# Kernel optimization log

Measured on AMD Instinct MI355X. Metric: run time of the kernel, lower is better.

Reference implementation:

```python
import jax, jax.numpy as jnp
from jax import lax
import numpy as np

B = 256
# conv stack: (in_ch, out_ch, kernel)
_CONV_CFG = [(1, 3, 4), (3, 9, 4), (9, 12, 4), (12, 15, 4), (15, 15, 3)]
_FLAT = 15 * 4 ** 4  # 3840, matches nn.Linear(15*(18-14)**4, 100)


def _conv4d(x, w, b):
    """True 4D valid convolution. x: [B,C,d1,d2,d3,d4], w: [O,I,k,k,k,k]."""
    dn = lax.conv_dimension_numbers(x.shape, w.shape, ('NCDHWX', 'OIDHWX', 'NCDHWX'))
    y = lax.conv_general_dilated(x, w, window_strides=(1, 1, 1, 1),
                                 padding='VALID', dimension_numbers=dn)
    return y + b.reshape((1, -1) + (1,) * 4)


def setup_inputs() -> dict:
    key = jax.random.key(0)
    ks = jax.random.split(key, 16)
    inp = {'x': jax.random.normal(ks[0], (B, 1, 18, 18, 18, 18), dtype=jnp.float32)}
    for i, (ci, co, k) in enumerate(_CONV_CFG, start=1):
        fan_in = ci * k ** 4
        inp[f'w{i}'] = jax.random.normal(ks[2 * i - 1], (co, ci, k, k, k, k), dtype=jnp.float32) / np.sqrt(fan_in)
        inp[f'b{i}'] = jnp.zeros((co,), dtype=jnp.float32)
    inp['fc1_w'] = jax.random.normal(ks[11], (_FLAT, 100), dtype=jnp.float32) / np.sqrt(_FLAT)
    inp['fc1_b'] = jnp.zeros((100,), dtype=jnp.float32)
    inp['fc2_w'] = jax.random.normal(ks[12], (100, 1), dtype=jnp.float32) / np.sqrt(100.0)
    inp['fc2_b'] = jnp.zeros((1,), dtype=jnp.float32)
    return inp


def reference(x, w1, b1, w2, b2, w3, b3, w4, b4, w5, b5, fc1_w, fc1_b, fc2_w, fc2_b):
    h = jax.nn.relu(_conv4d(x, w1, b1))
    h = jax.nn.relu(_conv4d(h, w2, b2))
    h = jax.nn.relu(_conv4d(h, w3, b3))
    h = jax.nn.relu(_conv4d(h, w4, b4))
    h = jax.nn.relu(_conv4d(h, w5, b5))  # [B,15,4,4,4,4]
    h = h.reshape(h.shape[0], -1)        # [B,3840], torch Flatten order
    # Dropout(0.5) is identity at inference (eval mode)
    h = jax.nn.relu(h @ fc1_w + fc1_b)
    return jax.nn.sigmoid(h @ fc2_w + fc2_b)  # [B,1]
```

## Files before the change

kernel.cpp:

```cpp
#include <hip/hip_runtime.h>
#include <hip/hip_bf16.h>


#define BATCH 256
typedef unsigned int u32;
typedef float    f32x4  __attribute__((ext_vector_type(4)));
typedef float    f32x16 __attribute__((ext_vector_type(16)));
typedef _Float16 f16x8  __attribute__((ext_vector_type(8)));

struct __attribute__((packed, aligned(4))) f16x8w { f16x8 v; };

__global__ void cvt_f32_f16(const float* __restrict__ in, _Float16* __restrict__ o, int n8) {
    int i = blockIdx.x * blockDim.x + threadIdx.x;
    if (i >= n8) return;
    const f32x4* p = (const f32x4*)(in + (size_t)i * 8);
    f32x4 a = p[0], b = p[1];
    f16x8 v;
    #pragma unroll
    for (int j = 0; j < 4; ++j) { v[j] = (_Float16)a[j]; v[4 + j] = (_Float16)b[j]; }
    *(f16x8*)(o + (size_t)i * 8) = v;
}

template<int COUT, int CIN, int KS, int S>
__global__ void prepack_v5(const float* __restrict__ w, _Float16* __restrict__ wf) {
    constexpr int STEPS = CIN * KS * 2 * KS;
    constexpr int TOT = STEPS * 512;
    int idx = blockIdx.x * 256 + threadIdx.x;
    if (idx >= TOT) return;
    int j    = idx & 7;
    int lane = (idx >> 3) & 63;
    int st   = idx >> 9;
    int k1 = st % KS;
    int r1 = st / KS;
    int k3p = r1 & 1;
    int r2  = r1 >> 1;
    int k2 = r2 % KS;
    int ci = r2 / KS;
    int gg = lane >> 5, col = lane & 31;
    int oc = col / S, s = col % S;
    int k3 = k3p * 2 + gg;
    int k4 = j - s;
    float v = 0.0f;
    if (oc < COUT && k3 < KS && k4 >= 0 && k4 < KS)
        v = w[((((oc * CIN + ci) * KS + k1) * KS + k2) * KS + k3) * KS + k4];
    wf[idx] = (_Float16)v;
}

template<int BYTES>
__device__ __forceinline__ void stage_b(const _Float16* gsrc, char* ldst, int tid) {
    constexpr int N16 = BYTES / 16;
    const int wv = tid >> 6, ln = tid & 63;
    #pragma unroll
    for (int it = 0; it * 256 < N16; ++it) {
        int u16 = it * 256 + (wv << 6);
        if (u16 < N16) {
            const char* gp = (const char*)gsrc + (size_t)(u16 + ln) * 16;
            __builtin_amdgcn_global_load_lds(
                (const __attribute__((address_space(1))) unsigned int*)gp,
                (__attribute__((address_space(3))) unsigned int*)(ldst + u16 * 16),
                16, 0, 0);
        }
    }
}

template<int CIN, int COUT, int KS, int DIN, int DP, int S, int OP, int T, int CG>
__launch_bounds__(256, 4)
__global__ void conv4d_v5(const _Float16* __restrict__ x,
                          const _Float16* __restrict__ wf,
                          const float* __restrict__ bias,
                          _Float16* __restrict__ out) {
    constexpr int DOUT = DIN - KS + 1;
    constexpr int NB   = (DOUT + S - 1) / S;
    constexpr int PCOL = DOUT * DOUT * NB;
    constexpr int NTC  = (PCOL + 31) / 32;
    constexpr int NG   = DOUT / T;
    static_assert(DOUT % T == 0, "T must divide DOUT");
    constexpr int XD2 = DIN * DP;
    constexpr int XD1 = DIN * XD2;
    constexpr int XCI = DIN * XD1;
    constexpr int GROUPS = CIN * KS * 2;
    static_assert(GROUPS % CG == 0, "CG must divide GROUPS");
    constexpr int CSTEPS = CG * KS;
    constexpr int CBYTES = CSTEPS * 1024;
    constexpr int NCHUNK = GROUPS / CG;
    constexpr int AJ = T + KS - 1;
    constexpr u32 NW   = (u32)BATCH * NG * NTC;
    constexpr u32 POUT = (u32)DOUT * DOUT * DOUT * OP;

    __shared__ char bsm[2 * CBYTES];
    const int tid = threadIdx.x;
    u32 wid = blockIdx.x * 4u + (u32)(tid >> 6);
    if (wid >= NW) wid = NW - 1u;
    const int ln = tid & 63;
    const int g  = ln >> 5;
    const int r  = ln & 31;

    u32 tc = wid % (u32)NTC;  u32 q = wid / (u32)NTC;
    u32 d1g = q % (u32)NG;    u32 b = q / (u32)NG;
    u32 rr = tc * 32u + (u32)r;  if (rr >= (u32)PCOL) rr = (u32)PCOL - 1u;
    u32 u  = rr % (u32)NB;    u32 q2 = rr / (u32)NB;
    u32 d3 = q2 % (u32)DOUT;  u32 d2 = q2 / (u32)DOUT;

    const u32 lanebase2 = (b * (u32)(CIN * XCI) + d1g * (u32)(T * XD1)
                         + d2 * (u32)XD2 + d3 * (u32)DP + (u32)(g * DP)
                         + u * (u32)S) * 2u;
    const char* xc = (const char*)x;

    f32x16 acc[T];
    #pragma unroll
    for (int t = 0; t < T; ++t)
        #pragma unroll
        for (int i = 0; i < 16; ++i) acc[t][i] = 0.0f;

    stage_b<CBYTES>(wf, &bsm[0], tid);

    #pragma unroll 1
    for (int ch = 0; ch < NCHUNK; ++ch) {
        __syncthreads();
        if (ch + 1 < NCHUNK)
            stage_b<CBYTES>(wf + (size_t)(ch + 1) * CSTEPS * 512,
                            &bsm[((ch + 1) & 1) * CBYTES], tid);
        const char* bb = &bsm[(ch & 1) * CBYTES] + ln * 16;
        #pragma unroll
        for (int gi = 0; gi < CG; ++gi) {
            int grp = ch * CG + gi;
            int k3p = grp & 1;
            int k2  = (grp >> 1) % KS;
            int ci  = (grp >> 1) / KS;
            u32 goff = ((u32)ci * (u32)XCI + (u32)k2 * (u32)XD2
                      + (u32)(k3p * 2 * DP)) * 2u;
            const char* ap = xc + lanebase2 + goff;
            f16x8 ar[AJ];
            #pragma unroll
            for (int j = 0; j < AJ; ++j)
                ar[j] = ((const f16x8w*)(ap + j * (XD1 * 2)))->v;
            #pragma unroll
            for (int k1 = 0; k1 < KS; ++k1) {
                f16x8 bf = *(const f16x8*)(bb + (gi * KS + k1) * 1024);
                #pragma unroll
                for (int t = 0; t < T; ++t)
                    acc[t] = __builtin_amdgcn_mfma_f32_32x32x16_f16(ar[k1 + t], bf, acc[t], 0, 0, 0);
            }
        }
    }

    const int oc = r / S, s = r % S;
    if (oc >= COUT) return;
    float bv = bias[oc];
    #pragma unroll
    for (int t = 0; t < T; ++t) {
        u32 d1 = d1g * (u32)T + (u32)t;
        #pragma unroll
        for (int reg = 0; reg < 16; ++reg) {
            int rowoff = (reg & 3) + 8 * (reg >> 2) + 4 * g;
            u32 rr2 = tc * 32u + (u32)rowoff;
            if (rr2 >= (u32)PCOL) rr2 = (u32)PCOL - 1u;
            u32 uu = rr2 % (u32)NB;  u32 qq = rr2 / (u32)NB;
            u32 dd3 = qq % (u32)DOUT; u32 dd2 = qq / (u32)DOUT;
            u32 d4 = uu * (u32)S + (u32)s;
            if (d4 < (u32)DOUT) {
                u32 oidx = (b * (u32)COUT + (u32)oc) * POUT
                         + ((d1 * (u32)DOUT + dd2) * (u32)DOUT + dd3) * (u32)OP + d4;
                out[oidx] = (_Float16)fmaxf(acc[t][reg] + bv, 0.0f);
            }
        }
    }
}

__global__ void prepack_fc1(const float* __restrict__ w, _Float16* __restrict__ wf) {
    int idx = blockIdx.x * 256 + threadIdx.x;
    if (idx >= 430080) return;
    int j    = idx & 7;
    int lane = (idx >> 3) & 63;
    int t9   = idx >> 9;
    int st   = t9 % 120;
    int ni   = t9 / 120;
    int k    = st * 32 + (lane >> 4) * 8 + j;
    int col  = ni * 16 + (lane & 15);
    wf[idx] = (_Float16)((col < 100) ? w[k * 100 + col] : 0.0f);
}

__launch_bounds__(256)
__global__ void fc1_mfma(const _Float16* __restrict__ h,
                         const _Float16* __restrict__ wfc,
                         const float* __restrict__ bias,
                         float* __restrict__ o) {
    int wv   = blockIdx.x * 4 + (threadIdx.x >> 6);
    int lane = threadIdx.x & 63;
    int r = lane & 15, g = lane >> 4;
    int mi = wv / 7, ni = wv % 7;
    const f16x8* A  = (const f16x8*)(h + (size_t)(mi * 16 + r) * 3840);
    const f16x8* Bv = (const f16x8*)wfc;
    f32x4 acc = {0.f, 0.f, 0.f, 0.f};
    #pragma unroll 4
    for (int st = 0; st < 120; ++st) {
        f16x8 a = A[st * 4 + g];
        f16x8 b = Bv[(ni * 120 + st) * 64 + lane];
        acc = __builtin_amdgcn_mfma_f32_16x16x32_f16(a, b, acc, 0, 0, 0);
    }
    int col = ni * 16 + r;
    if (col < 100) {
        float bv = bias[col];
        #pragma unroll
        for (int i = 0; i < 4; ++i) {
            int row = mi * 16 + g * 4 + i;
            o[row * 100 + col] = fmaxf(acc[i] + bv, 0.0f);
        }
    }
}

__global__ void fc2_sigmoid(const float* __restrict__ h,
                            const float* __restrict__ w,
                            const float* __restrict__ bias,
                            float* __restrict__ out) {
    int b = blockIdx.x * blockDim.x + threadIdx.x;
    if (b >= BATCH) return;
    const float* hb = h + b * 100;
    float acc = bias[0];
    #pragma unroll
    for (int j = 0; j < 100; ++j)
        acc = fmaf(hb[j], w[j], acc);
    out[b] = 1.0f / (1.0f + expf(-acc));
}

extern "C" void kernel_launch(void* const* d_in, const int* in_sizes, int n_in,
                              void* d_out, int out_size, void* d_ws, size_t ws_size,
                              hipStream_t stream) {
    const float* x    = (const float*)d_in[0];
    const float* w1   = (const float*)d_in[1];
    const float* b1   = (const float*)d_in[2];
    const float* w2   = (const float*)d_in[3];
    const float* b2   = (const float*)d_in[4];
    const float* w3   = (const float*)d_in[5];
    const float* b3   = (const float*)d_in[6];
    const float* w4   = (const float*)d_in[7];
    const float* b4   = (const float*)d_in[8];
    const float* w5   = (const float*)d_in[9];
    const float* b5   = (const float*)d_in[10];
    const float* fc1w = (const float*)d_in[11];
    const float* fc1b = (const float*)d_in[12];
    const float* fc2w = (const float*)d_in[13];
    const float* fc2b = (const float*)d_in[14];
    float* out = (float*)d_out;

    _Float16* W = (_Float16*)d_ws;
    size_t cur = 0;
    auto alloc = [&](size_t n) { _Float16* p = W + cur; cur += (n + 255) & ~(size_t)255; return p; };
    _Float16* x16 = alloc(26873856);
    _Float16* h1  = alloc(41472000);
    _Float16* h2  = alloc(47775744);
    _Float16* h3  = alloc(22394880);
    _Float16* h4  = alloc(4976640);
    _Float16* h5  = alloc(983040);
    _Float16* wf1 = alloc(16384);
    _Float16* wf2 = alloc(49152);
    _Float16* wf3 = alloc(147456);
    _Float16* wf4 = alloc(196608);
    _Float16* wf5 = alloc(138240);
    _Float16* wfc = alloc(430080);
    float* fc1out = (float*)alloc(51200 + 256);

    cvt_f32_f16<<<13122, 256, 0, stream>>>(x, x16, 3359232);

    prepack_v5<3, 1, 4, 4><<<64,  256, 0, stream>>>(w1, wf1);
    prepack_v5<9, 3, 4, 2><<<192, 256, 0, stream>>>(w2, wf2);
    prepack_v5<12, 9, 4, 2><<<576, 256, 0, stream>>>(w3, wf3);
    prepack_v5<15, 12, 4, 2><<<768, 256, 0, stream>>>(w4, wf4);
    prepack_v5<15, 15, 3, 2><<<540, 256, 0, stream>>>(w5, wf5);
    prepack_fc1<<<1680, 256, 0, stream>>>(fc1w, wfc);

    conv4d_v5<1, 3, 4, 18, 18, 4, 16, 3, 4><<<9280, 256, 0, stream>>>(x16, wf1, b1, h1);
    conv4d_v5<3, 9, 4, 15, 16, 2, 12, 3, 4><<<6912, 256, 0, stream>>>(h1, wf2, b2, h2);
    conv4d_v5<9, 12, 4, 12, 12, 2, 10, 3, 4><<<2496, 256, 0, stream>>>(h2, wf3, b3, h3);
    conv4d_v5<12, 15, 4, 9, 10, 2, 6, 3, 4><<<512, 256, 0, stream>>>(h3, wf4, b4, h4);
    conv4d_v5<15, 15, 3, 6, 6, 2, 4, 4, 6><<<64, 256, 0, stream>>>(h4, wf5, b5, h5);

    fc1_mfma<<<28, 256, 0, stream>>>(h5, wfc, fc1b, fc1out);
    fc2_sigmoid<<<1, 256, 0, stream>>>(fc1out, fc2w, fc2b, out);
}
```

Before: 996.0 us.

## Add 2D output tiling conv kernel reusing A fragments across d1 and d2

Adds a new conv4d_v6 kernel that tiles the output over two spatial dims (T1×T2) so each warp's loaded A fragments are reused across both k1 and k2 shifts. It also reorders the weight prepacking so weight chunks are staged per (ci,k3 pair) group. The aim is fewer global activation loads per MFMA and fewer blocks. The first four conv layers switch to it with new tile sizes. The cost is more accumulator registers per warp and dropping the occupancy hint from launch bounds, which may lower occupancy or cause spills.

```diff
diff --git a/kernel.cpp b/kernel.cpp
--- a/kernel.cpp
+++ b/kernel.cpp
@@ -19,6 +19,30 @@
     #pragma unroll
     for (int j = 0; j < 4; ++j) { v[j] = (_Float16)a[j]; v[4 + j] = (_Float16)b[j]; }
     *(f16x8*)(o + (size_t)i * 8) = v;
+}
+
+template<int COUT, int CIN, int KS, int S>
+__global__ void prepack_v6(const float* __restrict__ w, _Float16* __restrict__ wf) {
+    constexpr int STEPS = CIN * 2 * KS * KS;
+    constexpr int TOT = STEPS * 512;
+    int idx = blockIdx.x * 256 + threadIdx.x;
+    if (idx >= TOT) return;
+    int j    = idx & 7;
+    int lane = (idx >> 3) & 63;
+    int st   = idx >> 9;
+    int k1  = st % KS;
+    int k2  = (st / KS) % KS;
+    int sgv = st / (KS * KS);
+    int k3p = sgv & 1;
+    int ci  = sgv >> 1;
+    int gg = lane >> 5, col = lane & 31;
+    int oc = col / S, s = col % S;
+    int k3 = k3p * 2 + gg;
+    int k4 = j - s;
+    float v = 0.0f;
+    if (oc < COUT && k3 < KS && k4 >= 0 && k4 < KS)
+        v = w[((((oc * CIN + ci) * KS + k1) * KS + k2) * KS + k3) * KS + k4];
+    wf[idx] = (_Float16)v;
 }
 
 template<int COUT, int CIN, int KS, int S>
@@ -63,6 +87,131 @@
     }
 }
 
+template<int CIN, int COUT, int KS, int DIN, int DP, int S, int OP,
+         int T1, int T2, int CG>
+__launch_bounds__(256)
+__global__ void conv4d_v6(const _Float16* __restrict__ x,
+                          const _Float16* __restrict__ wf,
+                          const float* __restrict__ bias,
+                          _Float16* __restrict__ out) {
+    constexpr int DOUT = DIN - KS + 1;
+    constexpr int NB   = (DOUT + S - 1) / S;
+    static_assert((BATCH * DOUT * NB) % 32 == 0, "M rows must tile by 32");
+    static_assert(DOUT % T1 == 0 && DOUT % T2 == 0, "T must divide DOUT");
+    constexpr int NTC = BATCH * DOUT * NB / 32;
+    constexpr int NG1 = DOUT / T1;
+    constexpr int NG2 = DOUT / T2;
+    constexpr int XD2 = DIN * DP;
+    constexpr int XD1 = DIN * XD2;
+    constexpr int XCI = DIN * XD1;
+    constexpr int SG  = CIN * 2;
+    static_assert(SG % CG == 0, "CG must divide SG");
+    constexpr int NCHUNK = SG / CG;
+    constexpr int CBYTES = CG * KS * KS * 1024;
+    constexpr int AJ1 = T1 + KS - 1;
+    constexpr int AJ2 = T2 + KS - 1;
+    constexpr u32 POUT = (u32)DOUT * DOUT * DOUT * OP;
+
+    __shared__ char bsm[2 * CBYTES];
+    const int tid = threadIdx.x;
+    const u32 wid = blockIdx.x * 4u + (u32)(tid >> 6);
+    const int ln = tid & 63;
+    const int g  = ln >> 5;
+    const int r  = ln & 31;
+
+    u32 tc = wid / (u32)(NG1 * NG2);
+    u32 rm = wid % (u32)(NG1 * NG2);
+    u32 g1 = rm / (u32)NG2;
+    u32 g2 = rm % (u32)NG2;
+
+    u32 rr = tc * 32u + (u32)r;
+    u32 u  = rr % (u32)NB;   u32 q = rr / (u32)NB;
+    u32 d3 = q % (u32)DOUT;  u32 bb = q / (u32)DOUT;
+
+    const u32 lanebase2 = (bb * (u32)(CIN * XCI) + g1 * (u32)(T1 * XD1)
+                         + g2 * (u32)(T2 * XD2) + d3 * (u32)DP + (u32)(g * DP)
+                         + u * (u32)S) * 2u;
+    const char* xc = (const char*)x;
+
+    f32x16 acc[T1][T2];
+    #pragma unroll
+    for (int t1 = 0; t1 < T1; ++t1)
+        #pragma unroll
+        for (int t2 = 0; t2 < T2; ++t2)
+            #pragma unroll
+            for (int i = 0; i < 16; ++i) acc[t1][t2][i] = 0.0f;
+
+    stage_b<CBYTES>(wf, &bsm[0], tid);
+
+    #pragma unroll 1
+    for (int ch = 0; ch < NCHUNK; ++ch) {
+        __syncthreads();
+        if (ch + 1 < NCHUNK)
+            stage_b<CBYTES>(wf + (size_t)(ch + 1) * (CBYTES / 2),
+                            &bsm[((ch + 1) & 1) * CBYTES], tid);
+        const char* bb_lds = &bsm[(ch & 1) * CBYTES] + ln * 16;
+        #pragma unroll
+        for (int cgi = 0; cgi < CG; ++cgi) {
+            int sg  = ch * CG + cgi;
+            int k3p = sg & 1;
+            int ci  = sg >> 1;
+            u32 sgoff = ((u32)ci * (u32)XCI + (u32)(k3p * 2) * (u32)DP) * 2u;
+            const char* ap = xc + lanebase2 + sgoff;
+
+            f16x8 fr[AJ1][AJ2];
+            #pragma unroll
+            for (int j2 = 0; j2 < T2 - 1; ++j2)
+                #pragma unroll
+                for (int j1 = 0; j1 < AJ1; ++j1)
+                    fr[j1][j2] = ((const f16x8w*)(ap + (j1 * XD1 + j2 * XD2) * 2))->v;
+
+            #pragma unroll
+            for (int k2 = 0; k2 < KS; ++k2) {
+                constexpr int dummy = 0; (void)dummy;
+                const int jc = k2 + T2 - 1;
+                #pragma unroll
+                for (int j1 = 0; j1 < AJ1; ++j1)
+                    fr[j1][jc] = ((const f16x8w*)(ap + (j1 * XD1 + jc * XD2) * 2))->v;
+                #pragma unroll
+                for (int k1 = 0; k1 < KS; ++k1) {
+                    f16x8 bf = *(const f16x8*)(bb_lds + ((cgi * KS + k2) * KS + k1) * 1024);
+                    #pragma unroll
+                    for (int t1 = 0; t1 < T1; ++t1)
+                        #pragma unroll
+                        for (int t2 = 0; t2 < T2; ++t2)
+                            acc[t1][t2] = __builtin_amdgcn_mfma_f32_32x32x16_f16(
+                                fr[k1 + t1][k2 + t2], bf, acc[t1][t2], 0, 0, 0);
+                }
+            }
+        }
+    }
+
+    const int oc = r / S, s = r % S;
+    if (oc >= COUT) return;
+    float bv = bias[oc];
+    #pragma unroll
+    for (int t1 = 0; t1 < T1; ++t1) {
+        u32 d1 = g1 * (u32)T1 + (u32)t1;
+        #pragma unroll
+        for (int t2 = 0; t2 < T2; ++t2) {
+            u32 d2 = g2 * (u32)T2 + (u32)t2;
+            #pragma unroll
+            for (int reg = 0; reg < 16; ++reg) {
+                int rowoff = (reg & 3) + 8 * (reg >> 2) + 4 * g;
+                u32 rr2 = tc * 32u + (u32)rowoff;
+                u32 uu = rr2 % (u32)NB;  u32 qq = rr2 / (u32)NB;
+                u32 dd3 = qq % (u32)DOUT; u32 bb2 = qq / (u32)DOUT;
+                u32 d4 = uu * (u32)S + (u32)s;
+                if (d4 < (u32)DOUT) {
+                    u32 oidx = (bb2 * (u32)COUT + (u32)oc) * POUT
+                             + ((d1 * (u32)DOUT + d2) * (u32)DOUT + dd3) * (u32)OP + d4;
+                    out[oidx] = (_Float16)fmaxf(acc[t1][t2][reg] + bv, 0.0f);
+                }
+            }
+        }
+    }
+}
+
 template<int CIN, int COUT, int KS, int DIN, int DP, int S, int OP, int T, int CG>
 __launch_bounds__(256, 4)
 __global__ void conv4d_v5(const _Float16* __restrict__ x,
@@ -262,17 +411,17 @@
 
     cvt_f32_f16<<<13122, 256, 0, stream>>>(x, x16, 3359232);
 
-    prepack_v5<3, 1, 4, 4><<<64,  256, 0, stream>>>(w1, wf1);
-    prepack_v5<9, 3, 4, 2><<<192, 256, 0, stream>>>(w2, wf2);
-    prepack_v5<12, 9, 4, 2><<<576, 256, 0, stream>>>(w3, wf3);
-    prepack_v5<15, 12, 4, 2><<<768, 256, 0, stream>>>(w4, wf4);
+    prepack_v6<3, 1, 4, 4><<<64,  256, 0, stream>>>(w1, wf1);
+    prepack_v6<9, 3, 4, 2><<<192, 256, 0, stream>>>(w2, wf2);
+    prepack_v6<12, 9, 4, 2><<<576, 256, 0, stream>>>(w3, wf3);
+    prepack_v6<15, 12, 4, 2><<<768, 256, 0, stream>>>(w4, wf4);
     prepack_v5<15, 15, 3, 2><<<540, 256, 0, stream>>>(w5, wf5);
     prepack_fc1<<<1680, 256, 0, stream>>>(fc1w, wfc);
 
-    conv4d_v5<1, 3, 4, 18, 18, 4, 16, 3, 4><<<9280, 256, 0, stream>>>(x16, wf1, b1, h1);
-    conv4d_v5<3, 9, 4, 15, 16, 2, 12, 3, 4><<<6912, 256, 0, stream>>>(h1, wf2, b2, h2);
-    conv4d_v5<9, 12, 4, 12, 12, 2, 10, 3, 4><<<2496, 256, 0, stream>>>(h2, wf3, b3, h3);
-    conv4d_v5<12, 15, 4, 9, 10, 2, 6, 3, 4><<<512, 256, 0, stream>>>(h3, wf4, b4, h4);
+    conv4d_v6<1, 3, 4, 18, 18, 4, 16, 5, 1, 1><<<5400, 256, 0, stream>>>(x16, wf1, b1, h1);
+    conv4d_v6<3, 9, 4, 15, 16, 2, 12, 2, 2, 1><<<5184, 256, 0, stream>>>(h1, wf2, b2, h2);
+    conv4d_v6<9, 12, 4, 12, 12, 2, 10, 3, 3, 1><<<810, 256, 0, stream>>>(h2, wf3, b3, h3);
+    conv4d_v6<12, 15, 4, 9, 10, 2, 6, 2, 2, 2><<<324, 256, 0, stream>>>(h3, wf4, b4, h4);
     conv4d_v5<15, 15, 3, 6, 6, 2, 4, 4, 6><<<64, 256, 0, stream>>>(h4, wf5, b5, h5);
 
     fc1_mfma<<<28, 256, 0, stream>>>(h5, wfc, fc1b, fc1out);
```

After: 1.130 ms. +13.4%, slower.
